# Kernel tuning notes

Hardware: AMD Instinct MI355X
Metric: run time of the kernel (lower is better)

The kernel has to match this reference:

```python
import jax, jax.numpy as jnp
import numpy as np

EMBED_DIM = 1024
N1 = 4096
N2 = 4096


def setup_inputs() -> dict:
    key = jax.random.key(0)
    ks = jax.random.split(key, 14)
    s = 1.0 / np.sqrt(EMBED_DIM)
    def lin(k):
        kw, kb = jax.random.split(k)
        W = jax.random.uniform(kw, (EMBED_DIM, EMBED_DIM), jnp.float32, -s, s)
        b = jax.random.uniform(kb, (EMBED_DIM,), jnp.float32, -s, s)
        return W, b
    Wq1, bq1 = lin(ks[0]); Wk1, bk1 = lin(ks[1]); Wv1, bv1 = lin(ks[2])
    Wq2, bq2 = lin(ks[3]); Wk2, bk2 = lin(ks[4]); Wv2, bv2 = lin(ks[5])
    x1 = jax.random.normal(ks[6], (N1, EMBED_DIM), jnp.float32)
    x2 = jax.random.normal(ks[7], (N2, EMBED_DIM), jnp.float32)
    return {
        "input_tensor1": x1, "input_tensor2": x2,
        "Wq1": Wq1, "bq1": bq1, "Wk1": Wk1, "bk1": bk1, "Wv1": Wv1, "bv1": bv1,
        "Wq2": Wq2, "bq2": bq2, "Wk2": Wk2, "bk2": bk2, "Wv2": Wv2, "bv2": bv2,
    }


def reference(input_tensor1, input_tensor2,
              Wq1, bq1, Wk1, bk1, Wv1, bv1,
              Wq2, bq2, Wk2, bk2, Wv2, bv2):
    scale = 1.0 / jnp.sqrt(jnp.asarray(EMBED_DIM, input_tensor1.dtype))
    # torch Linear: y = x @ W.T + b
    q1 = input_tensor1 @ Wq1.T + bq1   # [N1, D]
    k1 = input_tensor1 @ Wk1.T + bk1
    v1 = input_tensor1 @ Wv1.T + bv1
    q2 = input_tensor2 @ Wq2.T + bq2   # [N2, D]
    k2 = input_tensor2 @ Wk2.T + bk2
    v2 = input_tensor2 @ Wv2.T + bv2
    # stream-2 queries attend over stream-1 keys/values
    scores1 = (q2 @ k1.T) * scale                  # [N2, N1]
    probs1 = jax.nn.softmax(scores1, axis=-1)      # dropout p=0 -> identity
    context1 = probs1 @ v1                         # [N2, D]
    # stream-1 queries attend over stream-2 keys/values
    scores2 = (q1 @ k2.T) * scale                  # [N1, N2]
    probs2 = jax.nn.softmax(scores2, axis=-1)
    context2 = probs2 @ v2                         # [N1, D]
    return (context1, context2)
```

## Files before the change

kernel.cpp:

```cpp
#include <hip/hip_runtime.h>
#include <hip/hip_bf16.h>
#include <cstdint>
#include <cstddef>

#define DEVINL __device__ __forceinline__

typedef __attribute__((ext_vector_type(4))) float   f32x4;
typedef __bf16 bf16x8 __attribute__((ext_vector_type(8)));
typedef __attribute__((ext_vector_type(4))) short   short4v;
typedef __attribute__((ext_vector_type(4))) float   float4v;

static constexpr int DIM = 1024;
static constexpr int NTOK = 4096;

DEVINL unsigned short f2bf(float f) {
  unsigned u = __float_as_uint(f);
  u += 0x7FFF + ((u >> 16) & 1);
  return (unsigned short)(u >> 16);
}
DEVINL float bf2f(unsigned short s) {
  return __uint_as_float(((unsigned)s) << 16);
}

DEVINL void gll16(const void* g, void* l) {
  __builtin_amdgcn_global_load_lds(
      (const __attribute__((address_space(1))) void*)g,
      (__attribute__((address_space(3))) void*)l, 16, 0, 0);
}

struct B3 { int bx, by, bz; };
DEVINL B3 xcd_remap(int GX, int GY, int GZ) {
  const int flat = blockIdx.x + GX * (blockIdx.y + GY * blockIdx.z);
  const int nwg  = GX * GY * GZ;
  const int chunk = nwg >> 3;
  const int vbid = (flat & 7) * chunk + (flat >> 3);
  B3 r;
  r.bx = vbid % GX;
  r.by = (vbid / GX) % GY;
  r.bz = vbid / (GX * GY);
  return r;
}

DEVINL void core128(const unsigned short* __restrict__ A, int lda,
                    const unsigned short* __restrict__ B, int ldb,
                    int K, int brow, int bcol, f32x4 acc[4][4])
{
  __shared__ unsigned short lds[16384];
  const int t = threadIdx.x;
  const int w = t >> 6, l = t & 63;
  const int wr = w >> 1, wc = w & 1;
  const int l15 = l & 15;
  const int srow = w * 16 + (l >> 2);
  const int scol = ((l & 3) ^ ((l >> 3) & 3)) << 3;
  const int cs = (((l >> 4) ^ ((l15 >> 1) & 3)) << 3);

  const unsigned short* aL = A + (size_t)(brow * 128 + srow) * lda + scol;
  const unsigned short* bL = B + (size_t)(bcol * 128 + srow) * ldb + scol;

#pragma unroll
  for (int m = 0; m < 4; ++m)
#pragma unroll
    for (int n = 0; n < 4; ++n) {
      f32x4 z = {0.f, 0.f, 0.f, 0.f};
      acc[m][n] = z;
    }

#define STAGE(buf, kt)                                                         \
  _Pragma("unroll")                                                            \
  for (int li = 0; li < 2; ++li) {                                             \
    gll16(aL + (size_t)(li * 64) * lda + (size_t)(kt) * 32,                    \
          lds + (buf) * 8192 + li * 2048 + w * 512);                           \
    gll16(bL + (size_t)(li * 64) * ldb + (size_t)(kt) * 32,                    \
          lds + (buf) * 8192 + 4096 + li * 2048 + w * 512);                    \
  }

#define BARR() do { asm volatile("" ::: "memory");                             \
                    __builtin_amdgcn_s_barrier();                              \
                    asm volatile("" ::: "memory"); } while (0)

  const int NT = K >> 5;

  STAGE(0, 0);
  asm volatile("s_waitcnt vmcnt(0)" ::: "memory");
  BARR();

  bf16x8 af[4], bfv[4];
  for (int kt = 0; kt < NT; ++kt) {
    const int cur = kt & 1;
    if (kt + 1 < NT) STAGE(cur ^ 1, kt + 1);

#pragma unroll
    for (int m = 0; m < 4; ++m)
      af[m] = *(const bf16x8*)(lds + cur * 8192 + (wr * 64 + m * 16 + l15) * 32 + cs);
#pragma unroll
    for (int n = 0; n < 4; ++n)
      bfv[n] = *(const bf16x8*)(lds + cur * 8192 + 4096 + (wc * 64 + n * 16 + l15) * 32 + cs);

    __builtin_amdgcn_s_setprio(1);
#pragma unroll
    for (int m = 0; m < 4; ++m)
#pragma unroll
      for (int n = 0; n < 4; ++n)
        acc[m][n] = __builtin_amdgcn_mfma_f32_16x16x32_bf16(af[m], bfv[n], acc[m][n], 0, 0, 0);
    __builtin_amdgcn_s_setprio(0);

    asm volatile("s_waitcnt vmcnt(0)" ::: "memory");
    BARR();
  }
#undef STAGE
#undef BARR
}

__global__ __launch_bounds__(256, 4)
void gemm128_scores(const unsigned short* __restrict__ A,
                    const unsigned short* __restrict__ B,
                    unsigned short* __restrict__ S, float scale)
{
  const B3 b = xcd_remap(32, 32, 1);
  f32x4 acc[4][4];
  core128(A, DIM, B, DIM, DIM, b.by, b.bx, acc);

  const int t = threadIdx.x, w = t >> 6, l = t & 63;
  const int wr = w >> 1, wc = w & 1;
  const int rr = (l >> 4) * 4, cc = l & 15;
#pragma unroll
  for (int m = 0; m < 4; ++m) {
    const int row0 = b.by * 128 + wr * 64 + m * 16 + rr;
#pragma unroll
    for (int n = 0; n < 4; ++n) {
      const int col = b.bx * 128 + wc * 64 + n * 16 + cc;
#pragma unroll
      for (int i = 0; i < 4; ++i)
        S[(size_t)(row0 + i) * NTOK + col] = f2bf(acc[m][n][i] * scale);
    }
  }
}

__global__ __launch_bounds__(256, 4)
void qkv128(const unsigned short* __restrict__ x1, const unsigned short* __restrict__ x2,
            const unsigned short* __restrict__ W6,
            const float* bq1, const float* bk1, const float* bv1,
            const float* bq2, const float* bk2, const float* bv2,
            unsigned short* q1, unsigned short* k1, unsigned short* v1T,
            unsigned short* q2, unsigned short* k2, unsigned short* v2T)
{
  const B3 b = xcd_remap(8, 32, 6);
  const int g = b.bz;
  const unsigned short* A = (g < 3) ? x1 : x2;
  const unsigned short* W = W6 + (size_t)g * (DIM * DIM);
  const float* bias = (g == 0) ? bq1 : (g == 1) ? bk1 : (g == 2) ? bv1
                    : (g == 3) ? bq2 : (g == 4) ? bk2 : bv2;
  unsigned short* out = (g == 0) ? q1 : (g == 1) ? k1 : (g == 2) ? v1T
                      : (g == 3) ? q2 : (g == 4) ? k2 : v2T;
  const bool vT = (g == 2 || g == 5);

  f32x4 acc[4][4];
  core128(A, DIM, W, DIM, DIM, b.by, b.bx, acc);

  const int t = threadIdx.x, w = t >> 6, l = t & 63;
  const int wr = w >> 1, wc = w & 1;
  const int rr = (l >> 4) * 4, cc = l & 15;

  if (!vT) {
#pragma unroll
    for (int m = 0; m < 4; ++m) {
      const int row0 = b.by * 128 + wr * 64 + m * 16 + rr;
#pragma unroll
      for (int n = 0; n < 4; ++n) {
        const int col = b.bx * 128 + wc * 64 + n * 16 + cc;
        const float bv_ = bias[col];
#pragma unroll
        for (int i = 0; i < 4; ++i)
          out[(size_t)(row0 + i) * DIM + col] = f2bf(acc[m][n][i] + bv_);
      }
    }
  } else {
#pragma unroll
    for (int m = 0; m < 4; ++m) {
      const int row0 = b.by * 128 + wr * 64 + m * 16 + rr;
#pragma unroll
      for (int n = 0; n < 4; ++n) {
        const int col = b.bx * 128 + wc * 64 + n * 16 + cc;
        const float bv_ = bias[col];
        short4v pk;
#pragma unroll
        for (int i = 0; i < 4; ++i) pk[i] = (short)f2bf(acc[m][n][i] + bv_);
        *(short4v*)(out + (size_t)col * NTOK + row0) = pk;
      }
    }
  }
}

__global__ __launch_bounds__(256, 4)
void pv128(const unsigned short* __restrict__ S1,
           const unsigned short* __restrict__ S2,
           const unsigned short* __restrict__ vTcat,
           float* __restrict__ out, float* __restrict__ P)
{
  const B3 b = xcd_remap(16, 32, 2);
  const int bx = b.bx, by = b.by, z = b.bz;
  const unsigned short* A = ((bx < 8) ? S1 : S2) + (size_t)z * 2048;
  const unsigned short* B = vTcat + (size_t)z * 2048;

  f32x4 acc[4][4];
  core128(A, NTOK, B, NTOK, 2048, by, bx, acc);

  const int t = threadIdx.x, w = t >> 6, l = t & 63;
  const int wr = w >> 1, wc = w & 1;
  const int rr = (l >> 4) * 4, cc = l & 15;
#pragma unroll
  for (int m = 0; m < 4; ++m) {
    const int row0 = by * 128 + wr * 64 + m * 16 + rr;
#pragma unroll
    for (int n = 0; n < 4; ++n) {
      const int cg = bx * 128 + wc * 64 + n * 16 + cc;
#pragma unroll
      for (int i = 0; i < 4; ++i) {
        const int r = row0 + i;
        if (z) {
          P[(size_t)r * 2048 + cg] = acc[m][n][i];
        } else {
          float* dst = (cg < 1024) ? (out + (size_t)r * 1024 + cg)
                                   : (out + 4194304 + (size_t)r * 1024 + (cg - 1024));
          *dst = acc[m][n][i];
        }
      }
    }
  }
}

__global__ __launch_bounds__(256)
void add_pv(float* __restrict__ out, const float* __restrict__ P)
{
  const int idx = blockIdx.x * 256 + threadIdx.x;
  const int r  = idx >> 9;
  const int c4 = (idx & 511) << 2;
  const float4v p = *(const float4v*)(P + (size_t)r * 2048 + c4);
  float* dst = (c4 < 1024) ? (out + (size_t)r * 1024 + c4)
                           : (out + 4194304 + (size_t)r * 1024 + (c4 - 1024));
  float4v a = *(const float4v*)dst;
#pragma unroll
  for (int j = 0; j < 4; ++j) a[j] += p[j];
  *(float4v*)dst = a;
}

__global__ __launch_bounds__(256)
void softmax_inplace(unsigned short* __restrict__ S)
{
  const int row = blockIdx.x;
  unsigned short* r = S + (size_t)row * NTOK;
  const int t = threadIdx.x, wave = t >> 6, lane = t & 63;
  __shared__ float red[4];

  bf16x8 d0 = *(const bf16x8*)(r + t * 8);
  bf16x8 d1 = *(const bf16x8*)(r + 2048 + t * 8);
  float v[16];
  {
    const unsigned short* p0 = (const unsigned short*)&d0;
    const unsigned short* p1 = (const unsigned short*)&d1;
#pragma unroll
    for (int j = 0; j < 8; ++j) { v[j] = bf2f(p0[j]); v[8 + j] = bf2f(p1[j]); }
  }
  float mx = v[0];
#pragma unroll
  for (int j = 1; j < 16; ++j) mx = fmaxf(mx, v[j]);
#pragma unroll
  for (int o = 32; o > 0; o >>= 1) mx = fmaxf(mx, __shfl_xor(mx, o));
  if (lane == 0) red[wave] = mx;
  __syncthreads();
  mx = fmaxf(fmaxf(red[0], red[1]), fmaxf(red[2], red[3]));

  float s = 0.f;
#pragma unroll
  for (int j = 0; j < 16; ++j) { v[j] = __expf(v[j] - mx); s += v[j]; }
#pragma unroll
  for (int o = 32; o > 0; o >>= 1) s += __shfl_xor(s, o);
  __syncthreads();
  if (lane == 0) red[wave] = s;
  __syncthreads();
  s = red[0] + red[1] + red[2] + red[3];
  const float inv = 1.0f / s;

  unsigned short o0[8], o1[8];
#pragma unroll
  for (int j = 0; j < 8; ++j) { o0[j] = f2bf(v[j] * inv); o1[j] = f2bf(v[8 + j] * inv); }
  *(bf16x8*)(r + t * 8)        = *(const bf16x8*)o0;
  *(bf16x8*)(r + 2048 + t * 8) = *(const bf16x8*)o1;
}

__global__ __launch_bounds__(256)
void cvt2(const float* __restrict__ a, const float* __restrict__ b,
          unsigned short* __restrict__ oa, unsigned short* __restrict__ ob)
{
  const float* in = blockIdx.y ? b : a;
  unsigned short* out = blockIdx.y ? ob : oa;
  const size_t i = ((size_t)blockIdx.x * 256 + threadIdx.x) * 4;
  float4v x = *(const float4v*)(in + i);
  short4v o;
#pragma unroll
  for (int j = 0; j < 4; ++j) o[j] = (short)f2bf(x[j]);
  *(short4v*)(out + i) = o;
}

__global__ __launch_bounds__(256)
void cvt_w(const float* w0, const float* w1, const float* w2,
           const float* w3, const float* w4, const float* w5,
           unsigned short* __restrict__ W6)
{
  const float* srcs[6] = {w0, w1, w2, w3, w4, w5};
  const float* in = srcs[blockIdx.y];
  unsigned short* out = W6 + (size_t)blockIdx.y * (DIM * DIM);
  const size_t i = ((size_t)blockIdx.x * 256 + threadIdx.x) * 4;
  float4v x = *(const float4v*)(in + i);
  short4v o;
#pragma unroll
  for (int j = 0; j < 4; ++j) o[j] = (short)f2bf(x[j]);
  *(short4v*)(out + i) = o;
}

extern "C" void kernel_launch(void* const* d_in, const int* in_sizes, int n_in,
                              void* d_out, int out_size, void* d_ws, size_t ws_size,
                              hipStream_t stream)
{
  const float* x1  = (const float*)d_in[0];
  const float* x2  = (const float*)d_in[1];
  const float* Wq1 = (const float*)d_in[2];  const float* bq1 = (const float*)d_in[3];
  const float* Wk1 = (const float*)d_in[4];  const float* bk1 = (const float*)d_in[5];
  const float* Wv1 = (const float*)d_in[6];  const float* bv1 = (const float*)d_in[7];
  const float* Wq2 = (const float*)d_in[8];  const float* bq2 = (const float*)d_in[9];
  const float* Wk2 = (const float*)d_in[10]; const float* bk2 = (const float*)d_in[11];
  const float* Wv2 = (const float*)d_in[12]; const float* bv2 = (const float*)d_in[13];
  float* out = (float*)d_out;

  unsigned short* ws  = (unsigned short*)d_ws;
  const size_t NTD = (size_t)NTOK * DIM;
  const size_t SM  = (size_t)NTOK * NTOK;
  unsigned short* x1b = ws;
  unsigned short* x2b = x1b + NTD;
  unsigned short* W6  = x2b + NTD;
  unsigned short* S1  = ws;
  unsigned short* S2  = ws + SM;
  unsigned short* q1  = ws + 2 * SM;
  unsigned short* k1  = q1 + NTD;
  unsigned short* q2  = k1 + NTD;
  unsigned short* k2  = q2 + NTD;
  unsigned short* vT  = k2 + NTD;
  unsigned short* v1T = vT;
  unsigned short* v2T = vT + NTD;
  float* P = (float*)q1;

  const dim3 blk(256);
  cvt2 <<<dim3(NTD / 1024, 2), blk, 0, stream>>>(x1, x2, x1b, x2b);
  cvt_w<<<dim3((DIM * DIM) / 1024, 6), blk, 0, stream>>>(Wq1, Wk1, Wv1, Wq2, Wk2, Wv2, W6);

  qkv128<<<dim3(8, 32, 6), blk, 0, stream>>>(
      x1b, x2b, W6, bq1, bk1, bv1, bq2, bk2, bv2, q1, k1, v1T, q2, k2, v2T);

  const float scale = 0.03125f;

  gemm128_scores<<<dim3(32, 32), blk, 0, stream>>>(q2, k1, S1, scale);
  softmax_inplace<<<dim3(NTOK), blk, 0, stream>>>(S1);
  gemm128_scores<<<dim3(32, 32), blk, 0, stream>>>(q1, k2, S2, scale);
  softmax_inplace<<<dim3(NTOK), blk, 0, stream>>>(S2);

  pv128<<<dim3(16, 32, 2), blk, 0, stream>>>(S1, S2, vT, out, P);
  add_pv<<<dim3(8192), blk, 0, stream>>>(out, P);
}
```

Before: 297.1 us.

## Enlarge GEMM block tile to 256x128 with 512 threads sharing B tile

Replaces the 128x128 GEMM core with a 256x128 tile computed by 8 waves. The two row halves share one staged B tile in LDS, so B global traffic per output drops and the grid has half as many blocks. Each wave keeps the same 64x64 accumulator footprint. LDS per block grows to 48KB, and a launch_bounds of 512x4 may constrain registers or occupancy. With fewer blocks, wave quantization across CUs also changes.

Result: faster. 275.7 us (-7.2%).

```diff
diff --git a/kernel.cpp b/kernel.cpp
--- a/kernel.cpp
+++ b/kernel.cpp
@@ -41,21 +41,20 @@
   return r;
 }
 
-DEVINL void core128(const unsigned short* __restrict__ A, int lda,
-                    const unsigned short* __restrict__ B, int ldb,
-                    int K, int brow, int bcol, f32x4 acc[4][4])
-{
-  __shared__ unsigned short lds[16384];
+DEVINL void core256x128(const unsigned short* __restrict__ A, int lda,
+                        const unsigned short* __restrict__ B, int ldb,
+                        int K, int brow, int bcol, f32x4 acc[4][4])
+{
+  __shared__ unsigned short lds[24576];
   const int t = threadIdx.x;
   const int w = t >> 6, l = t & 63;
   const int wr = w >> 1, wc = w & 1;
   const int l15 = l & 15;
-  const int srow = w * 16 + (l >> 2);
   const int scol = ((l & 3) ^ ((l >> 3) & 3)) << 3;
   const int cs = (((l >> 4) ^ ((l15 >> 1) & 3)) << 3);
 
-  const unsigned short* aL = A + (size_t)(brow * 128 + srow) * lda + scol;
-  const unsigned short* bL = B + (size_t)(bcol * 128 + srow) * ldb + scol;
+  const unsigned short* aL = A + (size_t)(brow * 256 + (l >> 2)) * lda + scol;
+  const unsigned short* bL = B + (size_t)(bcol * 128 + (l >> 2)) * ldb + scol;
 
 #pragma unroll
   for (int m = 0; m < 4; ++m)
@@ -66,12 +65,13 @@
     }
 
 #define STAGE(buf, kt)                                                         \
-  _Pragma("unroll")                                                            \
-  for (int li = 0; li < 2; ++li) {                                             \
-    gll16(aL + (size_t)(li * 64) * lda + (size_t)(kt) * 32,                    \
-          lds + (buf) * 8192 + li * 2048 + w * 512);                           \
-    gll16(bL + (size_t)(li * 64) * ldb + (size_t)(kt) * 32,                    \
-          lds + (buf) * 8192 + 4096 + li * 2048 + w * 512);                    \
+  {                                                                            \
+    gll16(aL + (size_t)(w * 16) * lda + (size_t)(kt) * 32,                     \
+          lds + (buf) * 12288 + w * 512);                                      \
+    gll16(aL + (size_t)(128 + w * 16) * lda + (size_t)(kt) * 32,               \
+          lds + (buf) * 12288 + 4096 + w * 512);                               \
+    gll16(bL + (size_t)(w * 16) * ldb + (size_t)(kt) * 32,                     \
+          lds + (buf) * 12288 + 8192 + w * 512);                               \
   }
 
 #define BARR() do { asm volatile("" ::: "memory");                             \
@@ -91,10 +91,10 @@
 
 #pragma unroll
     for (int m = 0; m < 4; ++m)
-      af[m] = *(const bf16x8*)(lds + cur * 8192 + (wr * 64 + m * 16 + l15) * 32 + cs);
+      af[m] = *(const bf16x8*)(lds + cur * 12288 + (wr * 64 + m * 16 + l15) * 32 + cs);
 #pragma unroll
     for (int n = 0; n < 4; ++n)
-      bfv[n] = *(const bf16x8*)(lds + cur * 8192 + 4096 + (wc * 64 + n * 16 + l15) * 32 + cs);
+      bfv[n] = *(const bf16x8*)(lds + cur * 12288 + 8192 + (wc * 64 + n * 16 + l15) * 32 + cs);
 
     __builtin_amdgcn_s_setprio(1);
 #pragma unroll
@@ -111,21 +111,21 @@
 #undef BARR
 }
 
-__global__ __launch_bounds__(256, 4)
-void gemm128_scores(const unsigned short* __restrict__ A,
-                    const unsigned short* __restrict__ B,
-                    unsigned short* __restrict__ S, float scale)
-{
-  const B3 b = xcd_remap(32, 32, 1);
+__global__ __launch_bounds__(512, 4)
+void gemm_scores(const unsigned short* __restrict__ A,
+                 const unsigned short* __restrict__ B,
+                 unsigned short* __restrict__ S, float scale)
+{
+  const B3 b = xcd_remap(32, 16, 1);
   f32x4 acc[4][4];
-  core128(A, DIM, B, DIM, DIM, b.by, b.bx, acc);
+  core256x128(A, DIM, B, DIM, DIM, b.by, b.bx, acc);
 
   const int t = threadIdx.x, w = t >> 6, l = t & 63;
   const int wr = w >> 1, wc = w & 1;
   const int rr = (l >> 4) * 4, cc = l & 15;
 #pragma unroll
   for (int m = 0; m < 4; ++m) {
-    const int row0 = b.by * 128 + wr * 64 + m * 16 + rr;
+    const int row0 = b.by * 256 + wr * 64 + m * 16 + rr;
 #pragma unroll
     for (int n = 0; n < 4; ++n) {
       const int col = b.bx * 128 + wc * 64 + n * 16 + cc;
@@ -136,15 +136,15 @@
   }
 }
 
-__global__ __launch_bounds__(256, 4)
-void qkv128(const unsigned short* __restrict__ x1, const unsigned short* __restrict__ x2,
-            const unsigned short* __restrict__ W6,
-            const float* bq1, const float* bk1, const float* bv1,
-            const float* bq2, const float* bk2, const float* bv2,
-            unsigned short* q1, unsigned short* k1, unsigned short* v1T,
-            unsigned short* q2, unsigned short* k2, unsigned short* v2T)
-{
-  const B3 b = xcd_remap(8, 32, 6);
+__global__ __launch_bounds__(512, 4)
+void qkv_gemm(const unsigned short* __restrict__ x1, const unsigned short* __restrict__ x2,
+              const unsigned short* __restrict__ W6,
+              const float* bq1, const float* bk1, const float* bv1,
+              const float* bq2, const float* bk2, const float* bv2,
+              unsigned short* q1, unsigned short* k1, unsigned short* v1T,
+              unsigned short* q2, unsigned short* k2, unsigned short* v2T)
+{
+  const B3 b = xcd_remap(8, 16, 6);
   const int g = b.bz;
   const unsigned short* A = (g < 3) ? x1 : x2;
   const unsigned short* W = W6 + (size_t)g * (DIM * DIM);
@@ -155,7 +155,7 @@
   const bool vT = (g == 2 || g == 5);
 
   f32x4 acc[4][4];
-  core128(A, DIM, W, DIM, DIM, b.by, b.bx, acc);
+  core256x128(A, DIM, W, DIM, DIM, b.by, b.bx, acc);
 
   const int t = threadIdx.x, w = t >> 6, l = t & 63;
   const int wr = w >> 1, wc = w & 1;
@@ -164,7 +164,7 @@
   if (!vT) {
 #pragma unroll
     for (int m = 0; m < 4; ++m) {
-      const int row0 = b.by * 128 + wr * 64 + m * 16 + rr;
+      const int row0 = b.by * 256 + wr * 64 + m * 16 + rr;
 #pragma unroll
       for (int n = 0; n < 4; ++n) {
         const int col = b.bx * 128 + wc * 64 + n * 16 + cc;
@@ -177,7 +177,7 @@
   } else {
 #pragma unroll
     for (int m = 0; m < 4; ++m) {
-      const int row0 = b.by * 128 + wr * 64 + m * 16 + rr;
+      const int row0 = b.by * 256 + wr * 64 + m * 16 + rr;
 #pragma unroll
       for (int n = 0; n < 4; ++n) {
         const int col = b.bx * 128 + wc * 64 + n * 16 + cc;
@@ -191,26 +191,26 @@
   }
 }
 
-__global__ __launch_bounds__(256, 4)
-void pv128(const unsigned short* __restrict__ S1,
-           const unsigned short* __restrict__ S2,
-           const unsigned short* __restrict__ vTcat,
-           float* __restrict__ out, float* __restrict__ P)
-{
-  const B3 b = xcd_remap(16, 32, 2);
+__global__ __launch_bounds__(512, 4)
+void pv_gemm(const unsigned short* __restrict__ S1,
+             const unsigned short* __restrict__ S2,
+             const unsigned short* __restrict__ vTcat,
+             float* __restrict__ out, float* __restrict__ P)
+{
+  const B3 b = xcd_remap(16, 16, 2);
   const int bx = b.bx, by = b.by, z = b.bz;
   const unsigned short* A = ((bx < 8) ? S1 : S2) + (size_t)z * 2048;
   const unsigned short* B = vTcat + (size_t)z * 2048;
 
   f32x4 acc[4][4];
-  core128(A, NTOK, B, NTOK, 2048, by, bx, acc);
+  core256x128(A, NTOK, B, NTOK, 2048, by, bx, acc);
 
   const int t = threadIdx.x, w = t >> 6, l = t & 63;
   const int wr = w >> 1, wc = w & 1;
   const int rr = (l >> 4) * 4, cc = l & 15;
 #pragma unroll
   for (int m = 0; m < 4; ++m) {
-    const int row0 = by * 128 + wr * 64 + m * 16 + rr;
+    const int row0 = by * 256 + wr * 64 + m * 16 + rr;
 #pragma unroll
     for (int n = 0; n < 4; ++n) {
       const int cg = bx * 128 + wc * 64 + n * 16 + cc;
@@ -353,16 +353,16 @@
   cvt2 <<<dim3(NTD / 1024, 2), blk, 0, stream>>>(x1, x2, x1b, x2b);
   cvt_w<<<dim3((DIM * DIM) / 1024, 6), blk, 0, stream>>>(Wq1, Wk1, Wv1, Wq2, Wk2, Wv2, W6);
 
-  qkv128<<<dim3(8, 32, 6), blk, 0, stream>>>(
+  qkv_gemm<<<dim3(8, 16, 6), dim3(512), 0, stream>>>(
       x1b, x2b, W6, bq1, bk1, bv1, bq2, bk2, bv2, q1, k1, v1T, q2, k2, v2T);
 
   const float scale = 0.03125f;
 
-  gemm128_scores<<<dim3(32, 32), blk, 0, stream>>>(q2, k1, S1, scale);
+  gemm_scores<<<dim3(32, 16), dim3(512), 0, stream>>>(q2, k1, S1, scale);
   softmax_inplace<<<dim3(NTOK), blk, 0, stream>>>(S1);
-  gemm128_scores<<<dim3(32, 32), blk, 0, stream>>>(q1, k2, S2, scale);
+  gemm_scores<<<dim3(32, 16), dim3(512), 0, stream>>>(q1, k2, S2, scale);
   softmax_inplace<<<dim3(NTOK), blk, 0, stream>>>(S2);
 
-  pv128<<<dim3(16, 32, 2), blk, 0, stream>>>(S1, S2, vT, out, P);
+  pv_gemm<<<dim3(16, 16, 2), dim3(512), 0, stream>>>(S1, S2, vT, out, P);
   add_pv<<<dim3(8192), blk, 0, stream>>>(out, P);
 }
```
